# Kernel tuning notes

Hardware: AMD Instinct MI355X
Metric: run time of the kernel (lower is better)

## Reference

```python
import jax, jax.numpy as jnp
import numpy as np

SH_C0 = 0.28209479177387814
EPS2D = 0.3      # gsplat low-pass filter added to 2D covariance diagonal
NEAR = 0.01
ALPHA_MIN = 1.0 / 255.0
ALPHA_MAX = 0.999


def setup_inputs() -> dict:
    key = jax.random.key(0)
    ks = jax.random.split(key, 5)
    N = 2048
    means = 0.1 * jax.random.normal(ks[0], (N, 3), jnp.float32)
    quats = jax.random.normal(ks[1], (N, 4), jnp.float32)
    scales = -2.3 + 0.3 * jax.random.normal(ks[2], (N, 3), jnp.float32)
    opacities = -1.0 + 0.5 * jax.random.normal(ks[3], (N,), jnp.float32)
    sh_coeffs = jax.random.normal(ks[4], (N, 1, 3), jnp.float32)
    viewmats = jnp.eye(4, dtype=jnp.float32).at[2, 3].set(2.0)[None]  # [1,4,4] world->cam
    Ks = jnp.array([[[150.0, 0.0, 64.0], [0.0, 150.0, 64.0], [0.0, 0.0, 1.0]]], jnp.float32)
    return dict(means=means, quats=quats, scales=scales, opacities=opacities,
                sh_coeffs=sh_coeffs, viewmats=viewmats, Ks=Ks, width=128, height=128)


def _splat_render(means, quats, scales, opacities, sh_coeffs, viewmats, Ks, width, height):
    # --- parameter activations (GaussianSplat.activated_parameters) ---
    quats = quats / jnp.linalg.norm(quats, axis=-1, keepdims=True)
    scales = jnp.minimum(jnp.exp(scales), 10.0)
    opac = jax.nn.sigmoid(opacities)                                  # [N]
    colors = jnp.maximum(sh_coeffs[:, 0, :] * SH_C0 + 0.5, 0.0)       # [N,3] sh_degree=0

    # --- 3D covariance from quaternion (w,x,y,z) and scale ---
    w, x, y, z = quats[:, 0], quats[:, 1], quats[:, 2], quats[:, 3]
    R = jnp.stack([
        1 - 2 * (y * y + z * z), 2 * (x * y - w * z), 2 * (x * z + w * y),
        2 * (x * y + w * z), 1 - 2 * (x * x + z * z), 2 * (y * z - w * x),
        2 * (x * z - w * y), 2 * (y * z + w * x), 1 - 2 * (x * x + y * y)],
        axis=-1).reshape(-1, 3, 3)                                    # [N,3,3]
    M = R * scales[:, None, :]                                        # R @ diag(s)
    cov3d = jnp.einsum('nij,nkj->nik', M, M)                          # [N,3,3]

    # --- project to camera frame ---
    Rcw = viewmats[:, :3, :3]                                         # [C,3,3]
    tcw = viewmats[:, :3, 3]                                          # [C,3]
    p_cam = jnp.einsum('cij,nj->cni', Rcw, means) + tcw[:, None, :]   # [C,N,3]
    Vc = jnp.einsum('cij,njk,clk->cnil', Rcw, cov3d, Rcw)             # [C,N,3,3]

    xc, yc, zc = p_cam[..., 0], p_cam[..., 1], p_cam[..., 2]
    valid = zc > NEAR
    zs = jnp.where(valid, zc, 1.0)
    rz = 1.0 / zs
    fx = Ks[:, 0, 0][:, None]; fy = Ks[:, 1, 1][:, None]
    cx = Ks[:, 0, 2][:, None]; cy = Ks[:, 1, 2][:, None]
    u = fx * xc * rz + cx                                             # [C,N]
    v = fy * yc * rz + cy

    # --- EWA 2D covariance: J Vc J^T + eps2d*I, J = d(proj)/d(p_cam) ---
    J00 = fx * rz; J02 = -fx * xc * rz * rz
    J11 = fy * rz; J12 = -fy * yc * rz * rz
    V00, V01, V02 = Vc[..., 0, 0], Vc[..., 0, 1], Vc[..., 0, 2]
    V11, V12, V22 = Vc[..., 1, 1], Vc[..., 1, 2], Vc[..., 2, 2]
    a = J00 * J00 * V00 + 2 * J00 * J02 * V02 + J02 * J02 * V22 + EPS2D
    b = J00 * (J11 * V01 + J12 * V02) + J02 * (J11 * V12 + J12 * V22)
    c = J11 * J11 * V11 + 2 * J11 * J12 * V12 + J12 * J12 * V22 + EPS2D
    det = a * c - b * b
    valid = valid & (det > 0)
    det_s = jnp.where(valid, det, 1.0)
    conA = c / det_s; conB = -b / det_s; conC = a / det_s             # conic (inverse cov)

    # --- per-pixel gaussian evaluation (pixel centers at +0.5) ---
    px = jnp.arange(width, dtype=jnp.float32) + 0.5                   # [W]
    py = jnp.arange(height, dtype=jnp.float32) + 0.5                  # [H]
    dx = px[None, None, :] - u[..., None]                             # [C,N,W]
    dy = py[None, None, :] - v[..., None]                             # [C,N,H]
    sigma = (0.5 * (conA[..., None, None] * (dx * dx)[:, :, None, :]
                    + conC[..., None, None] * (dy * dy)[..., None])
             + conB[..., None, None] * dy[..., None] * dx[:, :, None, :])  # [C,N,H,W]
    alpha = opac[None, :, None, None] * jnp.exp(-sigma)
    alpha = jnp.minimum(alpha, ALPHA_MAX)
    alpha = jnp.where(valid[..., None, None] & (alpha >= ALPHA_MIN), alpha, 0.0)

    # --- front-to-back alpha compositing in depth order ---
    order = jnp.argsort(jnp.where(valid, zc, jnp.inf), axis=1)        # [C,N]
    alpha_s = jnp.take_along_axis(alpha, order[:, :, None, None], axis=1)
    colors_s = jnp.take_along_axis(jnp.broadcast_to(colors[None], (alpha.shape[0],) + colors.shape),
                                   order[:, :, None], axis=1)         # [C,N,3]
    logT = jnp.cumsum(jnp.log1p(-alpha_s), axis=1)
    logT_excl = jnp.pad(logT, ((0, 0), (1, 0), (0, 0), (0, 0)))[:, :-1]
    weights = alpha_s * jnp.exp(logT_excl)                            # [C,N,H,W]
    img = jnp.einsum('cnhw,cnk->chwk', weights, colors_s)             # [C,H,W,3]
    return img


def reference(means, quats, scales, opacities, sh_coeffs, viewmats, Ks, width, height):
    return _splat_render(means, quats, scales, opacities, sh_coeffs, viewmats, Ks, width, height)
```

## Files before the change

### kernel.cpp

```cpp
#include <hip/hip_runtime.h>
#include <math.h>

#define SH_C0     0.28209479177387814f
#define EPS2D     0.3f
#define NEARZ     0.01f
#define ALPHA_MIN (1.0f/255.0f)
#define ALPHA_MAX 0.999f
#define LOG2E     1.4426950408889634f

#define SEGS   32
#define LSEG   8
#define NLAYER 4

__global__ __launch_bounds__(256) void prep_rank_kernel(
        const float* __restrict__ means,
        const float* __restrict__ quats,
        const float* __restrict__ scales,
        const float* __restrict__ opacities,
        const float* __restrict__ sh,
        const float* __restrict__ vm,
        const float* __restrict__ K,
        float* __restrict__ sorted,
        int N) {
    int wave = blockIdx.x * 4 + (threadIdx.x >> 6);
    int lane = threadIdx.x & 63;
    if (wave >= N) return;
    int i = wave;

    float r00=vm[0], r01=vm[1], r02=vm[2],  t0=vm[3];
    float r10=vm[4], r11=vm[5], r12=vm[6],  t1=vm[7];
    float r20=vm[8], r21=vm[9], r22=vm[10], t2=vm[11];

    float mx = means[3*i+0], my = means[3*i+1], mz = means[3*i+2];
    float zci = r20*mx + r21*my + r22*mz + t2;
    float keyi = (zci > NEARZ) ? zci : INFINITY;
    int cnt = 0;
    for (int j = lane; j < N; j += 64) {
        float ax = means[3*j+0], ay = means[3*j+1], az = means[3*j+2];
        float zcj = r20*ax + r21*ay + r22*az + t2;
        float keyj = (zcj > NEARZ) ? zcj : INFINITY;
        cnt += (keyj < keyi) || (keyj == keyi && j < i);
    }
    #pragma unroll
    for (int off = 32; off > 0; off >>= 1)
        cnt += __shfl_xor(cnt, off, 64);

    float qw = quats[4*i+0], qx = quats[4*i+1], qy = quats[4*i+2], qz = quats[4*i+3];
    float rqn = rsqrtf(qw*qw + qx*qx + qy*qy + qz*qz);
    qw *= rqn; qx *= rqn; qy *= rqn; qz *= rqn;

    float R00 = 1.f - 2.f*(qy*qy + qz*qz);
    float R01 = 2.f*(qx*qy - qw*qz);
    float R02 = 2.f*(qx*qz + qw*qy);
    float R10 = 2.f*(qx*qy + qw*qz);
    float R11 = 1.f - 2.f*(qx*qx + qz*qz);
    float R12 = 2.f*(qy*qz - qw*qx);
    float R20 = 2.f*(qx*qz - qw*qy);
    float R21 = 2.f*(qy*qz + qw*qx);
    float R22 = 1.f - 2.f*(qx*qx + qy*qy);

    float s0 = fminf(expf(scales[3*i+0]), 10.f);
    float s1 = fminf(expf(scales[3*i+1]), 10.f);
    float s2 = fminf(expf(scales[3*i+2]), 10.f);

    float M00=R00*s0, M01=R01*s1, M02=R02*s2;
    float M10=R10*s0, M11=R11*s1, M12=R12*s2;
    float M20=R20*s0, M21=R21*s1, M22=R22*s2;

    float c00 = M00*M00 + M01*M01 + M02*M02;
    float c01 = M00*M10 + M01*M11 + M02*M12;
    float c02 = M00*M20 + M01*M21 + M02*M22;
    float c11 = M10*M10 + M11*M11 + M12*M12;
    float c12 = M10*M20 + M11*M21 + M12*M22;
    float c22 = M20*M20 + M21*M21 + M22*M22;

    float xc = r00*mx + r01*my + r02*mz + t0;
    float yc = r10*mx + r11*my + r12*mz + t1;
    float zc = zci;

    float T00 = r00*c00 + r01*c01 + r02*c02;
    float T01 = r00*c01 + r01*c11 + r02*c12;
    float T02 = r00*c02 + r01*c12 + r02*c22;
    float T10 = r10*c00 + r11*c01 + r12*c02;
    float T11 = r10*c01 + r11*c11 + r12*c12;
    float T12 = r10*c02 + r11*c12 + r12*c22;
    float T20 = r20*c00 + r21*c01 + r22*c02;
    float T21 = r20*c01 + r21*c11 + r22*c12;
    float T22 = r20*c02 + r21*c12 + r22*c22;
    float V00 = T00*r00 + T01*r01 + T02*r02;
    float V01 = T00*r10 + T01*r11 + T02*r12;
    float V02 = T00*r20 + T01*r21 + T02*r22;
    float V11 = T10*r10 + T11*r11 + T12*r12;
    float V12 = T10*r20 + T11*r21 + T12*r22;
    float V22 = T20*r20 + T21*r21 + T22*r22;

    float fx = K[0], cx = K[2], fy = K[4], cy = K[5];

    bool valid = zc > NEARZ;
    float zs = valid ? zc : 1.0f;
    float rz = 1.0f / zs;
    float u = fx*xc*rz + cx;
    float v = fy*yc*rz + cy;
    float J00 = fx*rz;
    float J02 = -fx*xc*rz*rz;
    float J11 = fy*rz;
    float J12 = -fy*yc*rz*rz;

    float a = J00*J00*V00 + 2.f*J00*J02*V02 + J02*J02*V22 + EPS2D;
    float b = J00*(J11*V01 + J12*V02) + J02*(J11*V12 + J12*V22);
    float c = J11*J11*V11 + 2.f*J11*J12*V12 + J12*J12*V22 + EPS2D;
    float det = a*c - b*b;
    valid = valid && (det > 0.f);
    float det_s = valid ? det : 1.0f;
    float conA =  c / det_s;
    float conB = -b / det_s;
    float conC =  a / det_s;

    float op  = 1.0f / (1.0f + expf(-opacities[i]));
    float cr = fmaxf(sh[3*i+0]*SH_C0 + 0.5f, 0.f);
    float cg = fmaxf(sh[3*i+1]*SH_C0 + 0.5f, 0.f);
    float cb = fmaxf(sh[3*i+2]*SH_C0 + 0.5f, 0.f);

    float e0, e1, e2, e3, e4, e5;
    if (valid) {
        e0 = u; e1 = v;
        e2 = 0.5f*conA*LOG2E; e3 = conB*LOG2E; e4 = 0.5f*conC*LOG2E;
        e5 = op;
    } else {
        e0=0; e1=0; e2=0; e3=0; e4=0; e5=0;
    }

    if (lane < 12) {
        float val;
        switch (lane) {
            case 0:  val = e0; break;
            case 1:  val = e1; break;
            case 2:  val = e2; break;
            case 3:  val = e3; break;
            case 4:  val = e4; break;
            case 5:  val = e5; break;
            case 6:  val = cr; break;
            case 7:  val = cg; break;
            case 8:  val = cb; break;
            default: val = 0.f; break;
        }
        sorted[12*(size_t)cnt + lane] = val;
    }
}

__global__ __launch_bounds__(512, 8) void render_main_kernel(
        const float* __restrict__ sorted,
        float4* __restrict__ parts,
        int N, int P) {
    __shared__ float4 part[LSEG][64];
    int tid  = threadIdx.x;
    int lane = tid & 63;
    int w    = __builtin_amdgcn_readfirstlane(tid >> 6);
    int L    = blockIdx.x & (NLAYER - 1);
    int pg   = blockIdx.x >> 2;
    int p    = pg * 64 + lane;

    float px = (float)(p & 127) + 0.5f;
    float py = (float)(p >> 7) + 0.5f;

    int chunk = (N + SEGS - 1) / SEGS;
    int s  = L * LSEG + w;
    int g0 = s * chunk;
    int g1 = min(g0 + chunk, N);

    const float4* rec = (const float4*)sorted + 3*(size_t)g0;

    float accr = 0.f, accg = 0.f, accb = 0.f, T = 1.f;
    #pragma unroll 2
    for (int g = g0; g < g1; ++g) {
        float4 r0 = rec[0];
        float4 r1 = rec[1];
        float  cb = rec[2].x;
        rec += 3;
        float dx = px - r0.x, dy = py - r0.y;
        float t2 = fmaf(r0.z, dx, r0.w * dy);
        float m  = dx * t2;
        float arg = fmaf(-r1.x, dy*dy, -m);
        float al = r1.y * __builtin_amdgcn_exp2f(arg);
        al = fminf(al, ALPHA_MAX);
        al = (al >= ALPHA_MIN) ? al : 0.f;
        float wgt = T * al;
        accr = fmaf(wgt, r1.z, accr);
        accg = fmaf(wgt, r1.w, accg);
        accb = fmaf(wgt, cb,  accb);
        T = fmaf(-al, T, T);
    }
    part[w][lane] = make_float4(accr, accg, accb, T);
    __syncthreads();

    if (tid < 64) {
        float R = 0.f, G = 0.f, Bc = 0.f, Tr = 1.f;
        #pragma unroll
        for (int ss = 0; ss < LSEG; ++ss) {
            float4 q = part[ss][tid];
            R  = fmaf(Tr, q.x, R);
            G  = fmaf(Tr, q.y, G);
            Bc = fmaf(Tr, q.z, Bc);
            Tr *= q.w;
        }
        parts[(size_t)L * P + p] = make_float4(R, G, Bc, Tr);
    }
}

__global__ __launch_bounds__(256) void combine_kernel(
        const float4* __restrict__ parts,
        float* __restrict__ out, int P) {
    int p = blockIdx.x * 256 + threadIdx.x;
    if (p >= P) return;
    float R = 0.f, G = 0.f, B = 0.f, Tr = 1.f;
    #pragma unroll
    for (int l = 0; l < NLAYER; ++l) {
        float4 q = parts[(size_t)l * P + p];
        R  = fmaf(Tr, q.x, R);
        G  = fmaf(Tr, q.y, G);
        B  = fmaf(Tr, q.z, B);
        Tr *= q.w;
    }
    out[3*(size_t)p+0] = R;
    out[3*(size_t)p+1] = G;
    out[3*(size_t)p+2] = B;
}

extern "C" void kernel_launch(void* const* d_in, const int* in_sizes, int n_in,
                              void* d_out, int out_size, void* d_ws, size_t ws_size,
                              hipStream_t stream) {
    const float* means     = (const float*)d_in[0];
    const float* quats     = (const float*)d_in[1];
    const float* scales    = (const float*)d_in[2];
    const float* opacities = (const float*)d_in[3];
    const float* sh        = (const float*)d_in[4];
    const float* vm        = (const float*)d_in[5];
    const float* K         = (const float*)d_in[6];

    int N = in_sizes[0] / 3;
    int P = out_size / 3;

    float*  sorted = (float*)d_ws;
    float4* parts  = (float4*)((float*)d_ws + (size_t)N * 12);

    prep_rank_kernel<<<(N + 3) / 4, 256, 0, stream>>>(
        means, quats, scales, opacities, sh, vm, K, sorted, N);
    render_main_kernel<<<((P + 63) / 64) * NLAYER, 512, 0, stream>>>(
        sorted, parts, N, P);
    combine_kernel<<<(P + 255) / 256, 256, 0, stream>>>(
        parts, (float*)d_out, P);
}
```

Measured before the change: 96.55 us.

## Add per-gaussian bounding radii with 8x8 tile culling and fuse combine via atomics

The prep kernel now computes a conservative screen-space radius per gaussian, from where alpha drops below the minimum, and writes it into the sorted record. The render kernel maps each wave to an 8x8 pixel tile and skips gaussians whose box misses the tile, prefetching the next record header. The separate combine kernel is removed: the last layer block to finish a tile, detected with an atomic counter, composites and writes the output, and the counters are zeroed in the prep kernel. This saves exp work and a launch, but adds wave divergence, atomics and fences, and hardcodes a 128-wide image.

```diff
diff --git a/kernel.cpp b/kernel.cpp
--- a/kernel.cpp
+++ b/kernel.cpp
@@ -21,7 +21,13 @@
         const float* __restrict__ vm,
         const float* __restrict__ K,
         float* __restrict__ sorted,
-        int N) {
+        int* __restrict__ cnt,
+        int N, int tiles) {
+    if (blockIdx.x == 0) {
+        for (int t = threadIdx.x; t < tiles; t += 256) cnt[t] = 0;
+        if (threadIdx.x < 12) sorted[12*(size_t)N + threadIdx.x] = 0.f;
+    }
+
     int wave = blockIdx.x * 4 + (threadIdx.x >> 6);
     int lane = threadIdx.x & 63;
     if (wave >= N) return;
@@ -34,16 +40,16 @@
     float mx = means[3*i+0], my = means[3*i+1], mz = means[3*i+2];
     float zci = r20*mx + r21*my + r22*mz + t2;
     float keyi = (zci > NEARZ) ? zci : INFINITY;
-    int cnt = 0;
+    int cntk = 0;
     for (int j = lane; j < N; j += 64) {
         float ax = means[3*j+0], ay = means[3*j+1], az = means[3*j+2];
         float zcj = r20*ax + r21*ay + r22*az + t2;
         float keyj = (zcj > NEARZ) ? zcj : INFINITY;
-        cnt += (keyj < keyi) || (keyj == keyi && j < i);
+        cntk += (keyj < keyi) || (keyj == keyi && j < i);
     }
     #pragma unroll
     for (int off = 32; off > 0; off >>= 1)
-        cnt += __shfl_xor(cnt, off, 64);
+        cntk += __shfl_xor(cntk, off, 64);
 
     float qw = quats[4*i+0], qx = quats[4*i+1], qy = quats[4*i+2], qz = quats[4*i+3];
     float rqn = rsqrtf(qw*qw + qx*qx + qy*qy + qz*qz);
@@ -121,47 +127,62 @@
     float cg = fmaxf(sh[3*i+1]*SH_C0 + 0.5f, 0.f);
     float cb = fmaxf(sh[3*i+2]*SH_C0 + 0.5f, 0.f);
 
-    float e0, e1, e2, e3, e4, e5;
+    float e0=0,e1=0,eA=0,eB=0,eC=0,eOp=0,eR=0,eG=0,eBc=0,rx=0,ry=0;
     if (valid) {
-        e0 = u; e1 = v;
-        e2 = 0.5f*conA*LOG2E; e3 = conB*LOG2E; e4 = 0.5f*conC*LOG2E;
-        e5 = op;
-    } else {
-        e0=0; e1=0; e2=0; e3=0; e4=0; e5=0;
+        float qmax = log2f(op * 255.f);
+        if (qmax > 0.f) {
+            float a2 = 0.5f*conA*LOG2E;
+            float b2 = conB*LOG2E;
+            float c2 = 0.5f*conC*LOG2E;
+            float det2 = a2*c2 - 0.25f*b2*b2;
+            float inv = qmax / det2;
+            rx = sqrtf(c2 * inv) * 1.0001f + 0.01f;
+            ry = sqrtf(a2 * inv) * 1.0001f + 0.01f;
+            e0 = u; e1 = v; eA = a2; eB = b2; eC = c2; eOp = op;
+            eR = cr; eG = cg; eBc = cb;
+        }
     }
 
     if (lane < 12) {
         float val;
         switch (lane) {
-            case 0:  val = e0; break;
-            case 1:  val = e1; break;
-            case 2:  val = e2; break;
-            case 3:  val = e3; break;
-            case 4:  val = e4; break;
-            case 5:  val = e5; break;
-            case 6:  val = cr; break;
-            case 7:  val = cg; break;
-            case 8:  val = cb; break;
+            case 0:  val = e0;  break;
+            case 1:  val = e1;  break;
+            case 2:  val = rx;  break;
+            case 3:  val = ry;  break;
+            case 4:  val = eA;  break;
+            case 5:  val = eB;  break;
+            case 6:  val = eC;  break;
+            case 7:  val = eOp; break;
+            case 8:  val = eR;  break;
+            case 9:  val = eG;  break;
+            case 10: val = eBc; break;
             default: val = 0.f; break;
         }
-        sorted[12*(size_t)cnt + lane] = val;
+        sorted[12*(size_t)cntk + lane] = val;
     }
 }
 
 __global__ __launch_bounds__(512, 8) void render_main_kernel(
         const float* __restrict__ sorted,
         float4* __restrict__ parts,
+        int* __restrict__ cnt,
+        float* __restrict__ out,
         int N, int P) {
     __shared__ float4 part[LSEG][64];
     int tid  = threadIdx.x;
     int lane = tid & 63;
     int w    = __builtin_amdgcn_readfirstlane(tid >> 6);
     int L    = blockIdx.x & (NLAYER - 1);
-    int pg   = blockIdx.x >> 2;
-    int p    = pg * 64 + lane;
-
-    float px = (float)(p & 127) + 0.5f;
-    float py = (float)(p >> 7) + 0.5f;
+    int tile = blockIdx.x >> 2;
+    int tiles = P >> 6;
+
+    int tx = tile & 15, ty = tile >> 4;
+    float x0 = (float)(tx * 8) + 0.5f;
+    float y0 = (float)(ty * 8) + 0.5f;
+    float x1 = x0 + 7.f, y1 = y0 + 7.f;
+    float px = x0 + (float)(lane & 7);
+    float py = y0 + (float)(lane >> 3);
 
     int chunk = (N + SEGS - 1) / SEGS;
     int s  = L * LSEG + w;
@@ -171,24 +192,28 @@
     const float4* rec = (const float4*)sorted + 3*(size_t)g0;
 
     float accr = 0.f, accg = 0.f, accb = 0.f, T = 1.f;
-    #pragma unroll 2
-    for (int g = g0; g < g1; ++g) {
-        float4 r0 = rec[0];
-        float4 r1 = rec[1];
-        float  cb = rec[2].x;
-        rec += 3;
-        float dx = px - r0.x, dy = py - r0.y;
-        float t2 = fmaf(r0.z, dx, r0.w * dy);
-        float m  = dx * t2;
-        float arg = fmaf(-r1.x, dy*dy, -m);
-        float al = r1.y * __builtin_amdgcn_exp2f(arg);
-        al = fminf(al, ALPHA_MAX);
-        al = (al >= ALPHA_MIN) ? al : 0.f;
-        float wgt = T * al;
-        accr = fmaf(wgt, r1.z, accr);
-        accg = fmaf(wgt, r1.w, accg);
-        accb = fmaf(wgt, cb,  accb);
-        T = fmaf(-al, T, T);
+    float4 r0 = rec[0];
+    for (int g = g0; g < g1; ++g, rec += 3) {
+        float4 r0n = rec[3];
+        bool hit = (r0.y + r0.w >= y0) && (r0.y - r0.w <= y1) &&
+                   (r0.x + r0.z >= x0) && (r0.x - r0.z <= x1);
+        if (hit) {
+            float4 r1 = rec[1];
+            float4 r2 = rec[2];
+            float dx = px - r0.x, dy = py - r0.y;
+            float t2 = fmaf(r1.x, dx, r1.y * dy);
+            float m  = dx * t2;
+            float arg = fmaf(-r1.z, dy*dy, -m);
+            float al = r1.w * __builtin_amdgcn_exp2f(arg);
+            al = fminf(al, ALPHA_MAX);
+            al = (al >= ALPHA_MIN) ? al : 0.f;
+            float wgt = T * al;
+            accr = fmaf(wgt, r2.x, accr);
+            accg = fmaf(wgt, r2.y, accg);
+            accb = fmaf(wgt, r2.z, accb);
+            T = fmaf(-al, T, T);
+        }
+        r0 = r0n;
     }
     part[w][lane] = make_float4(accr, accg, accb, T);
     __syncthreads();
@@ -203,27 +228,28 @@
             Bc = fmaf(Tr, q.z, Bc);
             Tr *= q.w;
         }
-        parts[(size_t)L * P + p] = make_float4(R, G, Bc, Tr);
-    }
-}
-
-__global__ __launch_bounds__(256) void combine_kernel(
-        const float4* __restrict__ parts,
-        float* __restrict__ out, int P) {
-    int p = blockIdx.x * 256 + threadIdx.x;
-    if (p >= P) return;
-    float R = 0.f, G = 0.f, B = 0.f, Tr = 1.f;
-    #pragma unroll
-    for (int l = 0; l < NLAYER; ++l) {
-        float4 q = parts[(size_t)l * P + p];
-        R  = fmaf(Tr, q.x, R);
-        G  = fmaf(Tr, q.y, G);
-        B  = fmaf(Tr, q.z, B);
-        Tr *= q.w;
-    }
-    out[3*(size_t)p+0] = R;
-    out[3*(size_t)p+1] = G;
-    out[3*(size_t)p+2] = B;
+        parts[((size_t)L * tiles + tile) * 64 + tid] = make_float4(R, G, Bc, Tr);
+        __threadfence();
+        int old = 0;
+        if (tid == 0) old = atomicAdd(&cnt[tile], 1);
+        old = __shfl(old, 0, 64);
+        if (old == NLAYER - 1) {
+            __threadfence();
+            float R2 = 0.f, G2 = 0.f, B2 = 0.f, Tr2 = 1.f;
+            #pragma unroll
+            for (int l = 0; l < NLAYER; ++l) {
+                float4 q = parts[((size_t)l * tiles + tile) * 64 + tid];
+                R2 = fmaf(Tr2, q.x, R2);
+                G2 = fmaf(Tr2, q.y, G2);
+                B2 = fmaf(Tr2, q.z, B2);
+                Tr2 *= q.w;
+            }
+            int p = (ty * 8 + (tid >> 3)) * 128 + tx * 8 + (tid & 7);
+            out[3*(size_t)p+0] = R2;
+            out[3*(size_t)p+1] = G2;
+            out[3*(size_t)p+2] = B2;
+        }
+    }
 }
 
 extern "C" void kernel_launch(void* const* d_in, const int* in_sizes, int n_in,
@@ -239,14 +265,14 @@
 
     int N = in_sizes[0] / 3;
     int P = out_size / 3;
+    int tiles = P / 64;
 
     float*  sorted = (float*)d_ws;
-    float4* parts  = (float4*)((float*)d_ws + (size_t)N * 12);
+    float4* parts  = (float4*)((float*)d_ws + (size_t)(N+1) * 12);
+    int*    cnt    = (int*)(parts + (size_t)NLAYER * P);
 
     prep_rank_kernel<<<(N + 3) / 4, 256, 0, stream>>>(
-        means, quats, scales, opacities, sh, vm, K, sorted, N);
-    render_main_kernel<<<((P + 63) / 64) * NLAYER, 512, 0, stream>>>(
-        sorted, parts, N, P);
-    combine_kernel<<<(P + 255) / 256, 256, 0, stream>>>(
-        parts, (float*)d_out, P);
+        means, quats, scales, opacities, sh, vm, K, sorted, cnt, N, tiles);
+    render_main_kernel<<<tiles * NLAYER, 512, 0, stream>>>(
+        sorted, parts, cnt, (float*)d_out, N, P);
 }
```

After: 126.8 us. 1.31x slower.
